# Performance work log

Hardware: AMD Instinct MI355X
Metric: run time of the kernel (lower is better)

## Reference

```python
import jax, jax.numpy as jnp
import numpy as np

MARGIN = 0.2
EPS = 1e-8


def setup_inputs() -> dict:
    key = jax.random.key(0)
    k1, k2, k3 = jax.random.split(key, 3)
    B, D, T, C = 4096, 512, 65536, 100
    batch = jax.random.normal(k1, (B, D), dtype=jnp.float32)
    beta = jnp.ones((C,), dtype=jnp.float32) * 1.2  # learned per-class beta param
    labels = jax.random.randint(k2, (B,), 0, C)
    triplets = jax.random.randint(k3, (T, 3), 0, B)
    return {"batch": batch, "beta": beta, "labels": labels, "triplets": triplets}


def reference(batch, beta, labels, triplets):
    # Gather anchor / positive / negative embeddings: [T, D]
    a = batch[triplets[:, 0]]
    p = batch[triplets[:, 1]]
    n = batch[triplets[:, 2]]
    d_ap = jnp.sqrt(jnp.sum((a - p) ** 2, axis=-1) + EPS)  # [T]
    d_an = jnp.sqrt(jnp.sum((a - n) ** 2, axis=-1) + EPS)  # [T]
    b = beta[labels[triplets[:, 0]]]  # per-anchor-class beta, [T]
    pos_loss = jax.nn.relu(d_ap - b + MARGIN)
    neg_loss = jax.nn.relu(b - d_an + MARGIN)
    # torch bool+bool is logical OR; count triplets with any active hinge
    pair_count = jnp.sum(((pos_loss > 0.0) | (neg_loss > 0.0)).astype(jnp.float32))
    total = jnp.sum(pos_loss + neg_loss)
    loss = jnp.where(pair_count > 0.0, total / jnp.maximum(pair_count, 1.0), total)
    return loss
```

## Files before the change

### kernel.cpp

```cpp
#include <hip/hip_runtime.h>

#define MARGIN 0.2f
#define EPS_    1e-8f
#define BM 128
#define BK 64

typedef __attribute__((ext_vector_type(8))) short short8;
typedef __attribute__((ext_vector_type(4))) float f32x4;

__device__ __forceinline__ unsigned pack_bf16(float lo, float hi)
{
    union { float f; unsigned u; } a, b;
    a.f = lo; b.f = hi;
    unsigned ua = (a.u + 0x7fffu + ((a.u >> 16) & 1u)) >> 16;
    unsigned ub = (b.u + 0x7fffu + ((b.u >> 16) & 1u)) & 0xffff0000u;
    return ua | ub;
}

__global__ __launch_bounds__(256) void prep_kernel(
    const float* __restrict__ in, uint4* __restrict__ out, int n8,
    const float* __restrict__ beta, const int* __restrict__ labels,
    const int* __restrict__ trip, float* __restrict__ beta_tri, int T,
    float* __restrict__ ws_total, unsigned int* __restrict__ ws_cnt)
{
    int i = blockIdx.x * blockDim.x + threadIdx.x;
    if (i == 0) { *ws_total = 0.0f; *ws_cnt = 0u; }
    if (i < T) beta_tri[i] = beta[labels[trip[3 * i]]];
    if (i < n8) {
        const float4 a = ((const float4*)in)[2 * i + 0];
        const float4 b = ((const float4*)in)[2 * i + 1];
        uint4 r;
        r.x = pack_bf16(a.x, a.y);
        r.y = pack_bf16(a.z, a.w);
        r.z = pack_bf16(b.x, b.y);
        r.w = pack_bf16(b.z, b.w);
        out[i] = r;
    }
}

__global__ __launch_bounds__(256) void gemm_xxt(
    const char* __restrict__ xb,
    float* __restrict__ G, int B, int D)
{
    const int bm = blockIdx.y, bn = blockIdx.x;
    if (bn < bm) return;
    __shared__ char At[BM * BK * 2];
    __shared__ char Bt[BM * BK * 2];
    const int tid  = threadIdx.x;
    const int lane = tid & 63;
    const int w    = tid >> 6;
    const int wr   = w >> 1, wc = w & 1;
    const int rowb = D * 2;

    f32x4 acc[4][4] = {};

    const int nk = D / BK;
    for (int kk = 0; kk < nk; ++kk) {
        #pragma unroll
        for (int c4 = 0; c4 < 4; ++c4) {
            const int c = w * 4 + c4;
            const size_t arow = (size_t)bm * BM + c * 8 + (lane >> 3);
            const size_t brow = (size_t)bn * BM + c * 8 + (lane >> 3);
            const char* asrc = xb + arow * rowb + kk * (BK * 2) + (lane & 7) * 16;
            const char* bsrc = xb + brow * rowb + kk * (BK * 2) + (lane & 7) * 16;
            __builtin_amdgcn_global_load_lds((const unsigned*)asrc,
                (unsigned*)(At + c * 1024 + lane * 16), 16, 0, 0);
            __builtin_amdgcn_global_load_lds((const unsigned*)bsrc,
                (unsigned*)(Bt + c * 1024 + lane * 16), 16, 0, 0);
        }
        asm volatile("s_waitcnt vmcnt(0)" ::: "memory");
        __syncthreads();

        #pragma unroll
        for (int ks = 0; ks < 2; ++ks) {
            const int kbyte = ks * 64 + (lane >> 4) * 16;
            short8 a[4], b[4];
            #pragma unroll
            for (int m = 0; m < 4; ++m) {
                const int row = wr * 64 + m * 16 + (lane & 15);
                a[m] = *(const short8*)(At + row * 128 + kbyte);
            }
            #pragma unroll
            for (int n = 0; n < 4; ++n) {
                const int row = wc * 64 + n * 16 + (lane & 15);
                b[n] = *(const short8*)(Bt + row * 128 + kbyte);
            }
            #pragma unroll
            for (int m = 0; m < 4; ++m)
                #pragma unroll
                for (int n = 0; n < 4; ++n)
                    acc[m][n] = __builtin_amdgcn_mfma_f32_16x16x32_bf16(
                        a[m], b[n], acc[m][n], 0, 0, 0);
        }
        __syncthreads();
    }

    #pragma unroll
    for (int m = 0; m < 4; ++m)
        #pragma unroll
        for (int n = 0; n < 4; ++n)
            #pragma unroll
            for (int j = 0; j < 4; ++j) {
                const int row = bm * BM + wr * 64 + m * 16 + (lane >> 4) * 4 + j;
                const int col = bn * BM + wc * 64 + n * 16 + (lane & 15);
                G[(size_t)row * B + col] = acc[m][n][j];
            }
}

__global__ __launch_bounds__(256) void tri_eval(
    const float* __restrict__ G,
    const float* __restrict__ beta_tri,
    const int*   __restrict__ trip,
    int B, int T,
    float*        __restrict__ ws_total,
    unsigned int* __restrict__ ws_cnt)
{
    const int i = blockIdx.x * blockDim.x + threadIdx.x;
    float pn = 0.0f;
    int   c  = 0;
    if (i < T) {
        const int t0 = trip[3 * i + 0];
        const int t1 = trip[3 * i + 1];
        const int t2 = trip[3 * i + 2];
        const int r1 = t0 < t1 ? t0 : t1, c1 = t0 < t1 ? t1 : t0;
        const int r2 = t0 < t2 ? t0 : t2, c2 = t0 < t2 ? t2 : t0;
        const float g01 = G[(size_t)r1 * B + c1];
        const float g02 = G[(size_t)r2 * B + c2];
        const float n0  = G[(size_t)t0 * B + t0];
        const float n1  = G[(size_t)t1 * B + t1];
        const float n2  = G[(size_t)t2 * B + t2];
        const float b   = beta_tri[i];
        const float dap = sqrtf(fmaxf(n0 + n1 - 2.0f * g01, 0.0f) + EPS_);
        const float dan = sqrtf(fmaxf(n0 + n2 - 2.0f * g02, 0.0f) + EPS_);
        const float pos = fmaxf(dap - b + MARGIN, 0.0f);
        const float neg = fmaxf(b - dan + MARGIN, 0.0f);
        pn = pos + neg;
        c  = ((pos > 0.0f) || (neg > 0.0f)) ? 1 : 0;
    }
    #pragma unroll
    for (int off = 1; off < 64; off <<= 1) {
        pn += __shfl_xor(pn, off, 64);
        c  += __shfl_xor(c,  off, 64);
    }
    __shared__ float s_tot[4];
    __shared__ int   s_cnt[4];
    const int wid = threadIdx.x >> 6;
    if ((threadIdx.x & 63) == 0) { s_tot[wid] = pn; s_cnt[wid] = c; }
    __syncthreads();
    if (threadIdx.x == 0) {
        atomicAdd(ws_total, s_tot[0] + s_tot[1] + s_tot[2] + s_tot[3]);
        atomicAdd(ws_cnt, (unsigned)(s_cnt[0] + s_cnt[1] + s_cnt[2] + s_cnt[3]));
    }
}

__global__ __launch_bounds__(256) void triplet_loss_generic(
    const float* __restrict__ batch,
    const float* __restrict__ beta,
    const int*   __restrict__ labels,
    const int*   __restrict__ triplets,
    int T, int D,
    float*        __restrict__ ws_total,
    unsigned int* __restrict__ ws_cnt)
{
    const int lane   = threadIdx.x & 63;
    const int wid    = threadIdx.x >> 6;
    const int gwave  = (blockIdx.x * blockDim.x + threadIdx.x) >> 6;
    const int nwaves = (gridDim.x * blockDim.x) >> 6;
    const int dq     = D >> 2;

    float        tot = 0.0f;
    unsigned int cnt = 0u;

    for (int t = gwave; t < T; t += nwaves) {
        const int t0 = triplets[3 * t + 0];
        const int t1 = triplets[3 * t + 1];
        const int t2 = triplets[3 * t + 2];
        const float4* A = (const float4*)(batch + (size_t)t0 * D);
        const float4* P = (const float4*)(batch + (size_t)t1 * D);
        const float4* N = (const float4*)(batch + (size_t)t2 * D);
        float sap = 0.0f, san = 0.0f;
        for (int idx = lane; idx < dq; idx += 64) {
            const float4 av = A[idx];
            const float4 pv = P[idx];
            const float4 nv = N[idx];
            float dx = av.x - pv.x, dy = av.y - pv.y, dz = av.z - pv.z, dw = av.w - pv.w;
            sap += dx * dx + dy * dy + dz * dz + dw * dw;
            dx = av.x - nv.x; dy = av.y - nv.y; dz = av.z - nv.z; dw = av.w - nv.w;
            san += dx * dx + dy * dy + dz * dz + dw * dw;
        }
        #pragma unroll
        for (int off = 1; off < 64; off <<= 1) {
            sap += __shfl_xor(sap, off, 64);
            san += __shfl_xor(san, off, 64);
        }
        if (lane == 0) {
            const float d_ap = sqrtf(sap + EPS_);
            const float d_an = sqrtf(san + EPS_);
            const float b    = beta[labels[t0]];
            const float pos  = fmaxf(d_ap - b + MARGIN, 0.0f);
            const float neg  = fmaxf(b - d_an + MARGIN, 0.0f);
            tot += pos + neg;
            cnt += ((pos > 0.0f) || (neg > 0.0f)) ? 1u : 0u;
        }
    }

    __shared__ float        s_tot[4];
    __shared__ unsigned int s_cnt[4];
    if (lane == 0) { s_tot[wid] = tot; s_cnt[wid] = cnt; }
    __syncthreads();
    if (threadIdx.x == 0) {
        float        bt = 0.0f;
        unsigned int bc = 0u;
        const int nw = blockDim.x >> 6;
        for (int i = 0; i < nw; ++i) { bt += s_tot[i]; bc += s_cnt[i]; }
        atomicAdd(ws_total, bt);
        atomicAdd(ws_cnt, bc);
    }
}

__global__ void finalize_kernel(const float* __restrict__ ws_total,
                                const unsigned int* __restrict__ ws_cnt,
                                float* __restrict__ out)
{
    const float total = ws_total[0];
    const float pc    = (float)ws_cnt[0];
    out[0] = (pc > 0.0f) ? (total / fmaxf(pc, 1.0f)) : total;
}

extern "C" void kernel_launch(void* const* d_in, const int* in_sizes, int n_in,
                              void* d_out, int out_size, void* d_ws, size_t ws_size,
                              hipStream_t stream)
{
    const float* batch    = (const float*)d_in[0];
    const float* beta     = (const float*)d_in[1];
    const int*   labels   = (const int*)d_in[2];
    const int*   triplets = (const int*)d_in[3];

    const int B = in_sizes[2];
    const int D = in_sizes[0] / B;
    const int T = in_sizes[3] / 3;

    float*        ws_total = (float*)d_ws;
    unsigned int* ws_cnt   = (unsigned int*)((char*)d_ws + sizeof(float));

    const size_t hb_off = 32768;
    const size_t g_off  = (hb_off + (size_t)B * D * 2 + 255) & ~(size_t)255;
    const size_t bt_off = g_off + (size_t)B * B * 4;
    const size_t need   = bt_off + (size_t)T * 4;

    const bool fast = (B % BM == 0) && (D % BK == 0) && (ws_size >= need) && (T >= 1);

    if (fast) {
        uint4* hb       = (uint4*)((char*)d_ws + hb_off);
        float* G        = (float*)((char*)d_ws + g_off);
        float* beta_tri = (float*)((char*)d_ws + bt_off);

        const int n8 = (B * D) / 8;
        int pgrd = n8 > T ? n8 : T;
        prep_kernel<<<(pgrd + 255) / 256, 256, 0, stream>>>(
            batch, hb, n8, beta, labels, triplets, beta_tri, T, ws_total, ws_cnt);

        dim3 ggrid(B / BM, B / BM);
        gemm_xxt<<<ggrid, 256, 0, stream>>>((const char*)hb, G, B, D);

        tri_eval<<<(T + 255) / 256, 256, 0, stream>>>(
            G, beta_tri, triplets, B, T, ws_total, ws_cnt);
    } else {
        (void)hipMemsetAsync(d_ws, 0, 2 * sizeof(float), stream);
        const int block = 256;
        int grid = 2048;
        const int max_grid = (T + 3) / 4;
        if (grid > max_grid) grid = max_grid;
        triplet_loss_generic<<<grid, block, 0, stream>>>(
            batch, beta, labels, triplets, T, D, ws_total, ws_cnt);
    }

    finalize_kernel<<<1, 1, 0, stream>>>(ws_total, ws_cnt, (float*)d_out);
}
```

Measured before the change: 50.93 us.

## Double-buffer GEMM LDS tiles, launch only upper-triangle blocks, inline beta lookup

The Gram GEMM now double-buffers its LDS tiles, issuing the next K-slice's global-to-LDS loads before computing on the current one and waiting with a partial vmcnt. This is meant to overlap memory latency with MFMA work. The launch grid now covers only upper-triangular tile pairs, decoded from a linear block index, instead of a full 2D grid where half the blocks exit early. The per-triplet beta gather moves from the prep kernel into the triplet evaluation kernel, removing a workspace buffer. The costs are doubled LDS use, which may reduce occupancy, and a small loop per block to decode its tile index.

```diff
diff --git a/kernel.cpp b/kernel.cpp
--- a/kernel.cpp
+++ b/kernel.cpp
@@ -19,13 +19,10 @@
 
 __global__ __launch_bounds__(256) void prep_kernel(
     const float* __restrict__ in, uint4* __restrict__ out, int n8,
-    const float* __restrict__ beta, const int* __restrict__ labels,
-    const int* __restrict__ trip, float* __restrict__ beta_tri, int T,
     float* __restrict__ ws_total, unsigned int* __restrict__ ws_cnt)
 {
     int i = blockIdx.x * blockDim.x + threadIdx.x;
     if (i == 0) { *ws_total = 0.0f; *ws_cnt = 0u; }
-    if (i < T) beta_tri[i] = beta[labels[trip[3 * i]]];
     if (i < n8) {
         const float4 a = ((const float4*)in)[2 * i + 0];
         const float4 b = ((const float4*)in)[2 * i + 1];
@@ -40,12 +37,14 @@
 
 __global__ __launch_bounds__(256) void gemm_xxt(
     const char* __restrict__ xb,
-    float* __restrict__ G, int B, int D)
-{
-    const int bm = blockIdx.y, bn = blockIdx.x;
-    if (bn < bm) return;
-    __shared__ char At[BM * BK * 2];
-    __shared__ char Bt[BM * BK * 2];
+    float* __restrict__ G, int B, int D, int NB)
+{
+    int lin = blockIdx.x, bm = 0, rowlen = NB;
+    while (lin >= rowlen) { lin -= rowlen; ++bm; --rowlen; }
+    const int bn = bm + lin;
+
+    __shared__ char At[2][BM * BK * 2];
+    __shared__ char Bt[2][BM * BK * 2];
     const int tid  = threadIdx.x;
     const int lane = tid & 63;
     const int w    = tid >> 6;
@@ -54,8 +53,7 @@
 
     f32x4 acc[4][4] = {};
 
-    const int nk = D / BK;
-    for (int kk = 0; kk < nk; ++kk) {
+    auto stage = [&](int kk, int p) {
         #pragma unroll
         for (int c4 = 0; c4 < 4; ++c4) {
             const int c = w * 4 + c4;
@@ -64,12 +62,24 @@
             const char* asrc = xb + arow * rowb + kk * (BK * 2) + (lane & 7) * 16;
             const char* bsrc = xb + brow * rowb + kk * (BK * 2) + (lane & 7) * 16;
             __builtin_amdgcn_global_load_lds((const unsigned*)asrc,
-                (unsigned*)(At + c * 1024 + lane * 16), 16, 0, 0);
+                (unsigned*)(At[p] + c * 1024 + lane * 16), 16, 0, 0);
             __builtin_amdgcn_global_load_lds((const unsigned*)bsrc,
-                (unsigned*)(Bt + c * 1024 + lane * 16), 16, 0, 0);
-        }
-        asm volatile("s_waitcnt vmcnt(0)" ::: "memory");
-        __syncthreads();
+                (unsigned*)(Bt[p] + c * 1024 + lane * 16), 16, 0, 0);
+        }
+    };
+
+    const int nk = D / BK;
+    stage(0, 0);
+    for (int kk = 0; kk < nk; ++kk) {
+        const int p = kk & 1;
+        if (kk + 1 < nk) {
+            stage(kk + 1, p ^ 1);
+            asm volatile("s_waitcnt vmcnt(8)" ::: "memory");
+        } else {
+            asm volatile("s_waitcnt vmcnt(0)" ::: "memory");
+        }
+        __builtin_amdgcn_s_barrier();
+        __builtin_amdgcn_sched_barrier(0);
 
         #pragma unroll
         for (int ks = 0; ks < 2; ++ks) {
@@ -78,12 +88,12 @@
             #pragma unroll
             for (int m = 0; m < 4; ++m) {
                 const int row = wr * 64 + m * 16 + (lane & 15);
-                a[m] = *(const short8*)(At + row * 128 + kbyte);
+                a[m] = *(const short8*)(At[p] + row * 128 + kbyte);
             }
             #pragma unroll
             for (int n = 0; n < 4; ++n) {
                 const int row = wc * 64 + n * 16 + (lane & 15);
-                b[n] = *(const short8*)(Bt + row * 128 + kbyte);
+                b[n] = *(const short8*)(Bt[p] + row * 128 + kbyte);
             }
             #pragma unroll
             for (int m = 0; m < 4; ++m)
@@ -92,7 +102,9 @@
                     acc[m][n] = __builtin_amdgcn_mfma_f32_16x16x32_bf16(
                         a[m], b[n], acc[m][n], 0, 0, 0);
         }
-        __syncthreads();
+        asm volatile("s_waitcnt lgkmcnt(0)" ::: "memory");
+        __builtin_amdgcn_sched_barrier(0);
+        __builtin_amdgcn_s_barrier();
     }
 
     #pragma unroll
@@ -109,7 +121,8 @@
 
 __global__ __launch_bounds__(256) void tri_eval(
     const float* __restrict__ G,
-    const float* __restrict__ beta_tri,
+    const float* __restrict__ beta,
+    const int*   __restrict__ labels,
     const int*   __restrict__ trip,
     int B, int T,
     float*        __restrict__ ws_total,
@@ -129,7 +142,7 @@
         const float n0  = G[(size_t)t0 * B + t0];
         const float n1  = G[(size_t)t1 * B + t1];
         const float n2  = G[(size_t)t2 * B + t2];
-        const float b   = beta_tri[i];
+        const float b   = beta[labels[t0]];
         const float dap = sqrtf(fmaxf(n0 + n1 - 2.0f * g01, 0.0f) + EPS_);
         const float dan = sqrtf(fmaxf(n0 + n2 - 2.0f * g02, 0.0f) + EPS_);
         const float pos = fmaxf(dap - b + MARGIN, 0.0f);
@@ -245,26 +258,24 @@
 
     const size_t hb_off = 32768;
     const size_t g_off  = (hb_off + (size_t)B * D * 2 + 255) & ~(size_t)255;
-    const size_t bt_off = g_off + (size_t)B * B * 4;
-    const size_t need   = bt_off + (size_t)T * 4;
+    const size_t need   = g_off + (size_t)B * B * 4;
 
     const bool fast = (B % BM == 0) && (D % BK == 0) && (ws_size >= need) && (T >= 1);
 
     if (fast) {
-        uint4* hb       = (uint4*)((char*)d_ws + hb_off);
-        float* G        = (float*)((char*)d_ws + g_off);
-        float* beta_tri = (float*)((char*)d_ws + bt_off);
+        uint4* hb = (uint4*)((char*)d_ws + hb_off);
+        float* G  = (float*)((char*)d_ws + g_off);
 
         const int n8 = (B * D) / 8;
-        int pgrd = n8 > T ? n8 : T;
-        prep_kernel<<<(pgrd + 255) / 256, 256, 0, stream>>>(
-            batch, hb, n8, beta, labels, triplets, beta_tri, T, ws_total, ws_cnt);
-
-        dim3 ggrid(B / BM, B / BM);
-        gemm_xxt<<<ggrid, 256, 0, stream>>>((const char*)hb, G, B, D);
+        prep_kernel<<<(n8 + 255) / 256, 256, 0, stream>>>(
+            batch, hb, n8, ws_total, ws_cnt);
+
+        const int NB = B / BM;
+        const int nblk = NB * (NB + 1) / 2;
+        gemm_xxt<<<nblk, 256, 0, stream>>>((const char*)hb, G, B, D, NB);
 
         tri_eval<<<(T + 255) / 256, 256, 0, stream>>>(
-            G, beta_tri, triplets, B, T, ws_total, ws_cnt);
+            G, beta, labels, triplets, B, T, ws_total, ws_cnt);
     } else {
         (void)hipMemsetAsync(d_ws, 0, 2 * sizeof(float), stream);
         const int block = 256;
```

Result: faster. 49.91 us (-2.0%).
